# Kernel tuning notes

Hardware: AMD Instinct MI355X
Metric: run time of the kernel (lower is better)

Reference implementation:

```python
import jax, jax.numpy as jnp
import numpy as np

SCALE = 32.0 / 32.0  # alpha / rank
KEEP = 1.0 - 0.05    # dropout keep prob


def setup_inputs() -> dict:
    key = jax.random.key(0)
    kx, kw, ka, kb, km = jax.random.split(key, 5)
    B_, S, D_in, D_out, R = 4, 2048, 4096, 4096, 32
    x = jax.random.normal(kx, (B_, S, D_in), dtype=jnp.float32)
    W = jax.random.normal(kw, (D_out, D_in), dtype=jnp.float32) * (1.0 / np.sqrt(D_in))
    A = jax.random.normal(ka, (D_in, R), dtype=jnp.float32) * (1.0 / np.sqrt(D_in))
    Bm = jax.random.normal(kb, (R, D_out), dtype=jnp.float32) * 0.02
    # deterministic inverted-dropout mask: {0, 1/KEEP}
    drop_mask = (jax.random.uniform(km, (B_, S, D_in)) < KEEP).astype(jnp.float32) / KEEP
    return {"x": x, "W": W, "A": A, "B": Bm, "drop_mask": drop_mask}


def reference(x, W, A, B, drop_mask):
    # base: F.linear(x, W)  -> x @ W.T   [b,s,out]
    base = jnp.einsum("bsi,oi->bso", x, W)
    # lora: dropout(x) @ A @ B, low-rank path (contract rank first)
    lora = jnp.einsum("bsr,ro->bso", jnp.einsum("bsi,ir->bsr", x * drop_mask, A), B)
    return base + SCALE * lora
```

## Files before the change

kernel.cpp:

```cpp
#include <hip/hip_runtime.h>
#include <hip/hip_bf16.h>

typedef short bf16x8 __attribute__((ext_vector_type(8)));
typedef float f32x4  __attribute__((ext_vector_type(4)));

#define DIN  4096
#define DOUT 4096
#define MTOT 8192
#define RNK  32
#define NT   64

union Pk8 { __hip_bfloat16 h[8]; uint4 u; bf16x8 v; };

__device__ __forceinline__ uint4 pack8(float a0,float a1,float a2,float a3,
                                       float b0,float b1,float b2,float b3){
  Pk8 p;
  p.h[0]=__float2bfloat16(a0); p.h[1]=__float2bfloat16(a1);
  p.h[2]=__float2bfloat16(a2); p.h[3]=__float2bfloat16(a3);
  p.h[4]=__float2bfloat16(b0); p.h[5]=__float2bfloat16(b1);
  p.h[6]=__float2bfloat16(b2); p.h[7]=__float2bfloat16(b3);
  return p.u;
}
__device__ __forceinline__ bf16x8 pack8v(float a0,float a1,float a2,float a3,
                                         float b0,float b1,float b2,float b3){
  Pk8 p;
  p.h[0]=__float2bfloat16(a0); p.h[1]=__float2bfloat16(a1);
  p.h[2]=__float2bfloat16(a2); p.h[3]=__float2bfloat16(a3);
  p.h[4]=__float2bfloat16(b0); p.h[5]=__float2bfloat16(b1);
  p.h[6]=__float2bfloat16(b2); p.h[7]=__float2bfloat16(b3);
  return p.v;
}

__device__ __forceinline__ void gload_lds16(const void* g, void* l){
  __builtin_amdgcn_global_load_lds(
      (const __attribute__((address_space(1))) unsigned int*)g,
      (__attribute__((address_space(3))) unsigned int*)l, 16, 0, 0);
}

#define MFMA(A,B,C) __builtin_amdgcn_mfma_f32_16x16x32_bf16(A,B,C,0,0,0)
#define BAR   asm volatile("s_barrier" ::: "memory")
#define PRIO1 __builtin_amdgcn_s_setprio(1)
#define PRIO0 __builtin_amdgcn_s_setprio(0)

__global__ __launch_bounds__(256) void k_conv_w(const float* __restrict__ W,
                                                __hip_bfloat16* __restrict__ Wb){
  size_t i = ((size_t)blockIdx.x*256 + threadIdx.x) * 8;
  float4 a = *(const float4*)(W + i);
  float4 b = *(const float4*)(W + i + 4);
  *(uint4*)(Wb + i) = pack8(a.x,a.y,a.z,a.w,b.x,b.y,b.z,b.w);
}

__global__ __launch_bounds__(256) void k_conv_ab(const float* __restrict__ A,
                                                 const float* __restrict__ B,
                                                 __hip_bfloat16* __restrict__ At,
                                                 __hip_bfloat16* __restrict__ Bt){
  int idx = blockIdx.x*256 + threadIdx.x;
  if (idx < DIN*RNK){
    int k = idx >> 5, r = idx & 31;
    At[(size_t)r*DIN + k] = __float2bfloat16(A[(size_t)k*RNK + r]);
  } else {
    int j = idx - DIN*RNK;
    int n = j >> 5, k = j & 31;
    Bt[(size_t)n*RNK + k] = __float2bfloat16(B[(size_t)k*DOUT + n]);
  }
}

__global__ __launch_bounds__(256) void k_xt(const float* __restrict__ x,
                                            const float* __restrict__ mk,
                                            const __hip_bfloat16* __restrict__ At,
                                            __hip_bfloat16* __restrict__ xb,
                                            __hip_bfloat16* __restrict__ tb){
  __shared__ float sred[4*512];
  const int t = threadIdx.x, w = t >> 6, l = t & 63;
  const int r0 = blockIdx.x * 16;
  const int lane15 = l & 15, kb = l >> 4;
  const size_t rowbase = (size_t)(r0 + lane15) * DIN;
  const int kbase = w * 1024;

  f32x4 acc0 = {0.f,0.f,0.f,0.f}, acc1 = {0.f,0.f,0.f,0.f};
  const __hip_bfloat16* at0 = At + (size_t)lane15*DIN;
  const __hip_bfloat16* at1 = At + (size_t)(16+lane15)*DIN;

  #pragma unroll 2
  for (int kt = 0; kt < 32; ++kt){
    const int k0 = kbase + kt*32 + kb*8;
    float4 xa = *(const float4*)(x  + rowbase + k0);
    float4 xc = *(const float4*)(x  + rowbase + k0 + 4);
    float4 ma = *(const float4*)(mk + rowbase + k0);
    float4 mc = *(const float4*)(mk + rowbase + k0 + 4);
    *(uint4*)(xb + rowbase + k0) = pack8(xa.x,xa.y,xa.z,xa.w,xc.x,xc.y,xc.z,xc.w);
    bf16x8 af = pack8v(xa.x*ma.x,xa.y*ma.y,xa.z*ma.z,xa.w*ma.w,
                       xc.x*mc.x,xc.y*mc.y,xc.z*mc.z,xc.w*mc.w);
    bf16x8 b0 = *(const bf16x8*)(at0 + k0);
    bf16x8 b1 = *(const bf16x8*)(at1 + k0);
    acc0 = MFMA(af, b0, acc0);
    acc1 = MFMA(af, b1, acc1);
  }

  #pragma unroll
  for (int r = 0; r < 4; ++r){
    sred[(w*64+l)*8 + r]     = acc0[r];
    sred[(w*64+l)*8 + 4 + r] = acc1[r];
  }
  __syncthreads();
  #pragma unroll
  for (int e2 = 0; e2 < 2; ++e2){
    int e  = t*2 + e2;
    int el = e >> 3, er = e & 7;
    float s = sred[el*8+er] + sred[512+el*8+er] + sred[1024+el*8+er] + sred[1536+el*8+er];
    int col  = (er>>2)*16 + (el & 15);
    int orow = (el>>4)*4 + (er & 3);
    tb[(size_t)(r0 + orow)*RNK + col] = __float2bfloat16(s);
  }
}

__global__ __launch_bounds__(512, 2) void k_main2(const __hip_bfloat16* __restrict__ xb,
                                                  const __hip_bfloat16* __restrict__ Wb,
                                                  const __hip_bfloat16* __restrict__ tb,
                                                  const __hip_bfloat16* __restrict__ Bt,
                                                  float* __restrict__ out){
  __shared__ __align__(16) __hip_bfloat16 lds[65536];
  const int tid = threadIdx.x;
  const int l  = tid & 63, w = tid >> 6;
  const int wm = w >> 2,  wn = w & 3;
  const int lr = l & 15;
  const int ch = ((l >> 4) ^ ((l >> 1) & 3)) & 3;
  const int laneA = (wm*128 + lr)*32 + ch*8;
  const int laneB = (wn*64  + lr)*32 + ch*8;
  const int g_row = tid >> 2;
  const int g_ch  = (((tid & 3) ^ ((tid >> 3) & 3))) * 8;

  const int bid  = blockIdx.x;
  const int xcd  = bid & 7;
  const int idx  = bid >> 3;
  const int bm0  = (((xcd >> 1) << 3) + (idx & 7)) * 256;
  const int bn0  = (((xcd & 1) << 3) + (idx >> 3)) * 256;

  f32x4 acc[8][4];

  {
    const __hip_bfloat16* tp = tb + (size_t)(bm0 + wm*128 + lr)*RNK + (l>>4)*8;
    const __hip_bfloat16* bp = Bt + (size_t)(bn0 + wn*64  + lr)*RNK + (l>>4)*8;
    bf16x8 tf[8], bf[4];
    #pragma unroll
    for (int m = 0; m < 8; ++m) tf[m] = *(const bf16x8*)(tp + m*16*RNK);
    #pragma unroll
    for (int n = 0; n < 4; ++n) bf[n] = *(const bf16x8*)(bp + n*16*RNK);
    const f32x4 z = {0.f,0.f,0.f,0.f};
    #pragma unroll
    for (int m = 0; m < 8; ++m)
      #pragma unroll
      for (int n = 0; n < 4; ++n)
        acc[m][n] = MFMA(tf[m], bf[n], z);
  }
  asm volatile("" ::: "memory");

  auto STAGE = [&](int bb, int ab, int kh, int kt){
    const __hip_bfloat16* g = ab ? Wb : xb;
    const int base0 = ab ? bn0 : bm0;
    const int segb  = bb*32768 + ab*16384 + kh*8192;
    #pragma unroll
    for (int i = 0; i < 2; ++i){
      const __hip_bfloat16* src = g + (size_t)(base0 + i*128 + g_row)*DIN
                                    + kt*64 + kh*32 + g_ch;
      gload_lds16(src, (void*)&lds[segb + i*4096 + w*512]);
    }
  };

  STAGE(0,1,0,0); STAGE(0,0,0,0); STAGE(0,1,1,0); STAGE(0,0,1,0);
  STAGE(1,1,0,1); STAGE(1,0,0,1); STAGE(1,1,1,1);
  asm volatile("s_waitcnt vmcnt(6)" ::: "memory");
  BAR;

  #define LDV(off) (*(const bf16x8*)&lds[(off)])

  for (int t = 0; t < NT; ++t){
    const int b   = t & 1;
    const int sA0 = b*32768;
    const int sA1 = b*32768 + 8192;
    const int sB0 = b*32768 + 16384;
    const int sB1 = b*32768 + 24576;
    bf16x8 bk0[4], bk1[4];
    bf16x8 a0, a1, a2, a3;

    a0 = LDV(sA0+laneA);        a1 = LDV(sA0+laneA+512);
    a2 = LDV(sA0+laneA+1024);   a3 = LDV(sA0+laneA+1536);
    #pragma unroll
    for (int n = 0; n < 4; ++n) bk0[n] = LDV(sB0+laneB+n*512);
    if (t+1 < NT) STAGE(b^1, 0, 1, t+1);
    BAR;
    PRIO1;
    #pragma unroll
    for (int n = 0; n < 4; ++n){
      acc[0][n] = MFMA(a0, bk0[n], acc[0][n]);
      acc[1][n] = MFMA(a1, bk0[n], acc[1][n]);
      acc[2][n] = MFMA(a2, bk0[n], acc[2][n]);
      acc[3][n] = MFMA(a3, bk0[n], acc[3][n]);
    }
    PRIO0;
    BAR;

    a0 = LDV(sA0+laneA+2048);   a1 = LDV(sA0+laneA+2560);
    a2 = LDV(sA0+laneA+3072);   a3 = LDV(sA0+laneA+3584);
    #pragma unroll
    for (int n = 0; n < 4; ++n) bk1[n] = LDV(sB1+laneB+n*512);
    if (t+2 < NT) STAGE(b, 1, 0, t+2);
    BAR;
    PRIO1;
    #pragma unroll
    for (int n = 0; n < 4; ++n){
      acc[4][n] = MFMA(a0, bk0[n], acc[4][n]);
      acc[5][n] = MFMA(a1, bk0[n], acc[5][n]);
      acc[6][n] = MFMA(a2, bk0[n], acc[6][n]);
      acc[7][n] = MFMA(a3, bk0[n], acc[7][n]);
    }
    PRIO0;
    BAR;

    a0 = LDV(sA1+laneA);        a1 = LDV(sA1+laneA+512);
    a2 = LDV(sA1+laneA+1024);   a3 = LDV(sA1+laneA+1536);
    if (t+2 < NT) STAGE(b, 0, 0, t+2);
    BAR;
    PRIO1;
    #pragma unroll
    for (int n = 0; n < 4; ++n){
      acc[0][n] = MFMA(a0, bk1[n], acc[0][n]);
      acc[1][n] = MFMA(a1, bk1[n], acc[1][n]);
      acc[2][n] = MFMA(a2, bk1[n], acc[2][n]);
      acc[3][n] = MFMA(a3, bk1[n], acc[3][n]);
    }
    PRIO0;
    BAR;

    a0 = LDV(sA1+laneA+2048);   a1 = LDV(sA1+laneA+2560);
    a2 = LDV(sA1+laneA+3072);   a3 = LDV(sA1+laneA+3584);
    if (t+2 < NT) STAGE(b, 1, 1, t+2);
    BAR;
    PRIO1;
    #pragma unroll
    for (int n = 0; n < 4; ++n){
      acc[4][n] = MFMA(a0, bk1[n], acc[4][n]);
      acc[5][n] = MFMA(a1, bk1[n], acc[5][n]);
      acc[6][n] = MFMA(a2, bk1[n], acc[6][n]);
      acc[7][n] = MFMA(a3, bk1[n], acc[7][n]);
    }
    PRIO0;
    if (t < NT-2)       asm volatile("s_waitcnt vmcnt(6)" ::: "memory");
    else if (t == NT-2) asm volatile("s_waitcnt vmcnt(0)" ::: "memory");
    BAR;
  }

  const int orow = bm0 + wm*128 + (l>>4)*4;
  const int ocol = bn0 + wn*64  + (l&15);
  #pragma unroll
  for (int m = 0; m < 8; ++m)
    #pragma unroll
    for (int n = 0; n < 4; ++n)
      #pragma unroll
      for (int r = 0; r < 4; ++r)
        out[(size_t)(orow + m*16 + r)*DOUT + ocol + n*16] = acc[m][n][r];
  #undef LDV
}

__global__ void fb_t(const float* __restrict__ x, const float* __restrict__ mk,
                     const float* __restrict__ A, float* __restrict__ tf){
  const int m = blockIdx.x, t = threadIdx.x;
  float acc[RNK];
  #pragma unroll
  for (int r = 0; r < RNK; ++r) acc[r] = 0.f;
  for (int k = t; k < DIN; k += 256){
    float xm = x[(size_t)m*DIN + k] * mk[(size_t)m*DIN + k];
    #pragma unroll
    for (int r = 0; r < RNK; ++r) acc[r] += xm * A[(size_t)k*RNK + r];
  }
  #pragma unroll
  for (int r = 0; r < RNK; ++r){
    float v = acc[r];
    for (int o = 32; o; o >>= 1) v += __shfl_down(v, o);
    if ((t & 63) == 0) atomicAdd(&tf[(size_t)m*RNK + r], v);
  }
}

__global__ void fb_out(const float* __restrict__ x, const float* __restrict__ W,
                       const float* __restrict__ B, const float* __restrict__ tf,
                       float* __restrict__ out){
  size_t idx = (size_t)blockIdx.x*256 + threadIdx.x;
  int m = (int)(idx >> 12), n = (int)(idx & 4095);
  float acc = 0.f;
  for (int k = 0; k < DIN; ++k)
    acc += x[(size_t)m*DIN + k] * W[(size_t)n*DIN + k];
  #pragma unroll
  for (int r = 0; r < RNK; ++r)
    acc += tf[(size_t)m*RNK + r] * B[(size_t)r*DOUT + n];
  out[idx] = acc;
}

extern "C" void kernel_launch(void* const* d_in, const int* in_sizes, int n_in,
                              void* d_out, int out_size, void* d_ws, size_t ws_size,
                              hipStream_t stream) {
  const float* x  = (const float*)d_in[0];
  const float* W  = (const float*)d_in[1];
  const float* A  = (const float*)d_in[2];
  const float* B  = (const float*)d_in[3];
  const float* mk = (const float*)d_in[4];
  float* out = (float*)d_out;

  const size_t OFF_XB = 0;
  const size_t OFF_WB = OFF_XB + (size_t)MTOT*DIN*2;
  const size_t OFF_TB = OFF_WB + (size_t)DOUT*DIN*2;
  const size_t OFF_AT = OFF_TB + (size_t)MTOT*RNK*2;
  const size_t OFF_BT = OFF_AT + (size_t)RNK*DIN*2;
  const size_t NEED   = OFF_BT + (size_t)DIN*RNK*2;

  if (ws_size >= NEED){
    char* ws = (char*)d_ws;
    __hip_bfloat16* xb = (__hip_bfloat16*)(ws + OFF_XB);
    __hip_bfloat16* Wb = (__hip_bfloat16*)(ws + OFF_WB);
    __hip_bfloat16* tb = (__hip_bfloat16*)(ws + OFF_TB);
    __hip_bfloat16* At = (__hip_bfloat16*)(ws + OFF_AT);
    __hip_bfloat16* Bt = (__hip_bfloat16*)(ws + OFF_BT);

    k_conv_w <<<(DOUT*(size_t)DIN)/(256*8), 256, 0, stream>>>(W, Wb);
    k_conv_ab<<<(2*DIN*RNK)/256,            256, 0, stream>>>(A, B, At, Bt);
    k_xt     <<<MTOT/16,                    256, 0, stream>>>(x, mk, At, xb, tb);
    k_main2  <<<(MTOT/256)*(DOUT/256),      512, 0, stream>>>(xb, Wb, tb, Bt, out);
  } else {
    float* tf = (float*)d_ws;
    hipMemsetAsync(tf, 0, (size_t)MTOT*RNK*4, stream);
    fb_t  <<<MTOT, 256, 0, stream>>>(x, mk, A, tf);
    fb_out<<<((size_t)MTOT*DOUT)/256, 256, 0, stream>>>(x, W, B, tf, out);
  }
}
```

Before: 337.7 us.

## Software-pipeline LDS fragment loads with MFMAs and halve barriers per phase

Restructures the GEMM main loop so A and B fragments are double-buffered in registers (aE/aO, bk0/bk1). Each phase now loads the next phase's fragments from LDS while issuing MFMAs on the current ones, with a single barrier per phase instead of two. The prologue stages the whole second k-tile and preloads the first fragments, and sched_barrier stops the compiler from reordering across phase boundaries. The aim is to hide LDS read latency behind matrix math and cut barrier stalls, at the cost of higher register pressure. The tail waitcnt handling is simplified to an unconditional vmcnt(6), which may not drain the last in-flight tile before it is read.

```diff
diff --git a/kernel.cpp b/kernel.cpp
--- a/kernel.cpp
+++ b/kernel.cpp
@@ -39,6 +39,7 @@
 
 #define MFMA(A,B,C) __builtin_amdgcn_mfma_f32_16x16x32_bf16(A,B,C,0,0,0)
 #define BAR   asm volatile("s_barrier" ::: "memory")
+#define SB0   __builtin_amdgcn_sched_barrier(0)
 #define PRIO1 __builtin_amdgcn_s_setprio(1)
 #define PRIO0 __builtin_amdgcn_s_setprio(0)
 
@@ -167,87 +168,86 @@
     }
   };
 
+  #define ASEG(bb,kh) ((bb)*32768 + (kh)*8192)
+  #define BSEG(bb,kh) ((bb)*32768 + 16384 + (kh)*8192)
+  #define LDV(off) (*(const bf16x8*)&lds[(off)])
+
   STAGE(0,1,0,0); STAGE(0,0,0,0); STAGE(0,1,1,0); STAGE(0,0,1,0);
-  STAGE(1,1,0,1); STAGE(1,0,0,1); STAGE(1,1,1,1);
-  asm volatile("s_waitcnt vmcnt(6)" ::: "memory");
-  BAR;
-
-  #define LDV(off) (*(const bf16x8*)&lds[(off)])
+  STAGE(1,1,0,1); STAGE(1,0,0,1); STAGE(1,1,1,1); STAGE(1,0,1,1);
+  asm volatile("s_waitcnt vmcnt(8)" ::: "memory");
+  BAR; SB0;
+
+  bf16x8 aE[4], aO[4], bk0[4], bk1[4];
+  #pragma unroll
+  for (int i = 0; i < 4; ++i) aE[i] = LDV(ASEG(0,0)+laneA+i*512);
+  #pragma unroll
+  for (int n = 0; n < 4; ++n) bk0[n] = LDV(BSEG(0,0)+laneB+n*512);
 
   for (int t = 0; t < NT; ++t){
-    const int b   = t & 1;
-    const int sA0 = b*32768;
-    const int sA1 = b*32768 + 8192;
-    const int sB0 = b*32768 + 16384;
-    const int sB1 = b*32768 + 24576;
-    bf16x8 bk0[4], bk1[4];
-    bf16x8 a0, a1, a2, a3;
-
-    a0 = LDV(sA0+laneA);        a1 = LDV(sA0+laneA+512);
-    a2 = LDV(sA0+laneA+1024);   a3 = LDV(sA0+laneA+1536);
-    #pragma unroll
-    for (int n = 0; n < 4; ++n) bk0[n] = LDV(sB0+laneB+n*512);
-    if (t+1 < NT) STAGE(b^1, 0, 1, t+1);
-    BAR;
+    const int b = t & 1, bn = b ^ 1;
+
+    BAR; SB0;
+    #pragma unroll
+    for (int i = 0; i < 4; ++i) aO[i] = LDV(ASEG(b,0)+laneA+2048+i*512);
+    #pragma unroll
+    for (int n = 0; n < 4; ++n) bk1[n] = LDV(BSEG(b,1)+laneB+n*512);
+    if (t+2 < NT) STAGE(b, 1, 0, t+2);
     PRIO1;
     #pragma unroll
     for (int n = 0; n < 4; ++n){
-      acc[0][n] = MFMA(a0, bk0[n], acc[0][n]);
-      acc[1][n] = MFMA(a1, bk0[n], acc[1][n]);
-      acc[2][n] = MFMA(a2, bk0[n], acc[2][n]);
-      acc[3][n] = MFMA(a3, bk0[n], acc[3][n]);
+      acc[0][n] = MFMA(aE[0], bk0[n], acc[0][n]);
+      acc[1][n] = MFMA(aE[1], bk0[n], acc[1][n]);
+      acc[2][n] = MFMA(aE[2], bk0[n], acc[2][n]);
+      acc[3][n] = MFMA(aE[3], bk0[n], acc[3][n]);
     }
     PRIO0;
-    BAR;
-
-    a0 = LDV(sA0+laneA+2048);   a1 = LDV(sA0+laneA+2560);
-    a2 = LDV(sA0+laneA+3072);   a3 = LDV(sA0+laneA+3584);
-    #pragma unroll
-    for (int n = 0; n < 4; ++n) bk1[n] = LDV(sB1+laneB+n*512);
-    if (t+2 < NT) STAGE(b, 1, 0, t+2);
-    BAR;
+
+    BAR; SB0;
+    #pragma unroll
+    for (int i = 0; i < 4; ++i) aE[i] = LDV(ASEG(b,1)+laneA+i*512);
+    if (t+2 < NT) STAGE(b, 0, 0, t+2);
     PRIO1;
     #pragma unroll
     for (int n = 0; n < 4; ++n){
-      acc[4][n] = MFMA(a0, bk0[n], acc[4][n]);
-      acc[5][n] = MFMA(a1, bk0[n], acc[5][n]);
-      acc[6][n] = MFMA(a2, bk0[n], acc[6][n]);
-      acc[7][n] = MFMA(a3, bk0[n], acc[7][n]);
+      acc[4][n] = MFMA(aO[0], bk0[n], acc[4][n]);
+      acc[5][n] = MFMA(aO[1], bk0[n], acc[5][n]);
+      acc[6][n] = MFMA(aO[2], bk0[n], acc[6][n]);
+      acc[7][n] = MFMA(aO[3], bk0[n], acc[7][n]);
     }
     PRIO0;
-    BAR;
-
-    a0 = LDV(sA1+laneA);        a1 = LDV(sA1+laneA+512);
-    a2 = LDV(sA1+laneA+1024);   a3 = LDV(sA1+laneA+1536);
-    if (t+2 < NT) STAGE(b, 0, 0, t+2);
-    BAR;
+
+    BAR; SB0;
+    #pragma unroll
+    for (int i = 0; i < 4; ++i) aO[i] = LDV(ASEG(b,1)+laneA+2048+i*512);
+    if (t+2 < NT) STAGE(b, 1, 1, t+2);
     PRIO1;
     #pragma unroll
     for (int n = 0; n < 4; ++n){
-      acc[0][n] = MFMA(a0, bk1[n], acc[0][n]);
-      acc[1][n] = MFMA(a1, bk1[n], acc[1][n]);
-      acc[2][n] = MFMA(a2, bk1[n], acc[2][n]);
-      acc[3][n] = MFMA(a3, bk1[n], acc[3][n]);
+      acc[0][n] = MFMA(aE[0], bk1[n], acc[0][n]);
+      acc[1][n] = MFMA(aE[1], bk1[n], acc[1][n]);
+      acc[2][n] = MFMA(aE[2], bk1[n], acc[2][n]);
+      acc[3][n] = MFMA(aE[3], bk1[n], acc[3][n]);
     }
     PRIO0;
-    BAR;
-
-    a0 = LDV(sA1+laneA+2048);   a1 = LDV(sA1+laneA+2560);
-    a2 = LDV(sA1+laneA+3072);   a3 = LDV(sA1+laneA+3584);
-    if (t+2 < NT) STAGE(b, 1, 1, t+2);
-    BAR;
+    asm volatile("s_waitcnt vmcnt(6)" ::: "memory");
+
+    BAR; SB0;
+    if (t+1 < NT){
+      #pragma unroll
+      for (int i = 0; i < 4; ++i) aE[i] = LDV(ASEG(bn,0)+laneA+i*512);
+      #pragma unroll
+      for (int n = 0; n < 4; ++n) bk0[n] = LDV(BSEG(bn,0)+laneB+n*512);
+    }
+    if (t+2 < NT) STAGE(b, 0, 1, t+2);
     PRIO1;
     #pragma unroll
     for (int n = 0; n < 4; ++n){
-      acc[4][n] = MFMA(a0, bk1[n], acc[4][n]);
-      acc[5][n] = MFMA(a1, bk1[n], acc[5][n]);
-      acc[6][n] = MFMA(a2, bk1[n], acc[6][n]);
-      acc[7][n] = MFMA(a3, bk1[n], acc[7][n]);
+      acc[4][n] = MFMA(aO[0], bk1[n], acc[4][n]);
+      acc[5][n] = MFMA(aO[1], bk1[n], acc[5][n]);
+      acc[6][n] = MFMA(aO[2], bk1[n], acc[6][n]);
+      acc[7][n] = MFMA(aO[3], bk1[n], acc[7][n]);
     }
     PRIO0;
-    if (t < NT-2)       asm volatile("s_waitcnt vmcnt(6)" ::: "memory");
-    else if (t == NT-2) asm volatile("s_waitcnt vmcnt(0)" ::: "memory");
-    BAR;
   }
 
   const int orow = bm0 + wm*128 + (l>>4)*4;
@@ -260,6 +260,8 @@
       for (int r = 0; r < 4; ++r)
         out[(size_t)(orow + m*16 + r)*DOUT + ocol + n*16] = acc[m][n][r];
   #undef LDV
+  #undef ASEG
+  #undef BSEG
 }
 
 __global__ void fb_t(const float* __restrict__ x, const float* __restrict__ mk,
```

After: 337.2 us. Within noise of the previous version (-0.1%).

## Restructure main GEMM into 8-phase pipeline with new LDS swizzle and quadrant MFMA

Applied to the files above, without the earlier changes.

Rewrites the main bf16 GEMM loop to process two K-tiles per iteration as eight phases. Each phase computes one quadrant of the accumulator tile with full K=64 per LDS tile, and global-to-LDS staging is interleaved one segment per phase. The LDS layout changes to 64-element rows with an XOR swizzle across 8 chunks to cut bank conflicts. Explicit lgkmcnt/vmcnt waits and sched_barrier fences control instruction ordering. This adds more barriers per K-tile and keeps more fragments live in registers, which raises register pressure and tightens the prefetch-distance accounting.

```diff
diff --git a/kernel.cpp b/kernel.cpp
--- a/kernel.cpp
+++ b/kernel.cpp
@@ -9,6 +9,7 @@
 #define MTOT 8192
 #define RNK  32
 #define NT   64
+#define NT2  32
 
 union Pk8 { __hip_bfloat16 h[8]; uint4 u; bf16x8 v; };
 
@@ -39,6 +40,7 @@
 
 #define MFMA(A,B,C) __builtin_amdgcn_mfma_f32_16x16x32_bf16(A,B,C,0,0,0)
 #define BAR   asm volatile("s_barrier" ::: "memory")
+#define SB0   __builtin_amdgcn_sched_barrier(0)
 #define PRIO1 __builtin_amdgcn_s_setprio(1)
 #define PRIO0 __builtin_amdgcn_s_setprio(0)
 
@@ -114,7 +116,7 @@
   }
 }
 
-__global__ __launch_bounds__(512, 2) void k_main2(const __hip_bfloat16* __restrict__ xb,
+__global__ __launch_bounds__(512, 2) void k_main3(const __hip_bfloat16* __restrict__ xb,
                                                   const __hip_bfloat16* __restrict__ Wb,
                                                   const __hip_bfloat16* __restrict__ tb,
                                                   const __hip_bfloat16* __restrict__ Bt,
@@ -123,12 +125,13 @@
   const int tid = threadIdx.x;
   const int l  = tid & 63, w = tid >> 6;
   const int wm = w >> 2,  wn = w & 3;
-  const int lr = l & 15;
-  const int ch = ((l >> 4) ^ ((l >> 1) & 3)) & 3;
-  const int laneA = (wm*128 + lr)*32 + ch*8;
-  const int laneB = (wn*64  + lr)*32 + ch*8;
-  const int g_row = tid >> 2;
-  const int g_ch  = (((tid & 3) ^ ((tid >> 3) & 3))) * 8;
+  const int lr = l & 15, kb = l >> 4;
+  const int cSwz = (l & 7) ^ ((l >> 3) & 7);
+  const int pc   = lr*64 + (kb ^ (lr & 3))*8;
+  const int khp0 = ((lr >> 2) & 1) * 32;
+  const int khp1 = 32 - khp0;
+  const int aBase = wm*8192;
+  const int bBase = 16384 + wn*4096;
 
   const int bid  = blockIdx.x;
   const int xcd  = bid & 7;
@@ -139,8 +142,8 @@
   f32x4 acc[8][4];
 
   {
-    const __hip_bfloat16* tp = tb + (size_t)(bm0 + wm*128 + lr)*RNK + (l>>4)*8;
-    const __hip_bfloat16* bp = Bt + (size_t)(bn0 + wn*64  + lr)*RNK + (l>>4)*8;
+    const __hip_bfloat16* tp = tb + (size_t)(bm0 + wm*128 + lr)*RNK + kb*8;
+    const __hip_bfloat16* bp = Bt + (size_t)(bn0 + wn*64  + lr)*RNK + kb*8;
     bf16x8 tf[8], bf[4];
     #pragma unroll
     for (int m = 0; m < 8; ++m) tf[m] = *(const bf16x8*)(tp + m*16*RNK);
@@ -155,98 +158,63 @@
   }
   asm volatile("" ::: "memory");
 
-  auto STAGE = [&](int bb, int ab, int kh, int kt){
+  auto STAGE = [&](int buf, int ab, int h, int kt){
     const __hip_bfloat16* g = ab ? Wb : xb;
     const int base0 = ab ? bn0 : bm0;
-    const int segb  = bb*32768 + ab*16384 + kh*8192;
+    const int seg = buf*32768 + ab*16384 + h*8192;
     #pragma unroll
     for (int i = 0; i < 2; ++i){
-      const __hip_bfloat16* src = g + (size_t)(base0 + i*128 + g_row)*DIN
-                                    + kt*64 + kh*32 + g_ch;
-      gload_lds16(src, (void*)&lds[segb + i*4096 + w*512]);
+      const int row = i*64 + w*8 + (l >> 3);
+      const __hip_bfloat16* src = g + (size_t)(base0 + h*128 + row)*DIN
+                                    + kt*64 + cSwz*8;
+      gload_lds16(src, (void*)&lds[seg + i*4096 + w*512]);
     }
   };
 
-  STAGE(0,1,0,0); STAGE(0,0,0,0); STAGE(0,1,1,0); STAGE(0,0,1,0);
-  STAGE(1,1,0,1); STAGE(1,0,0,1); STAGE(1,1,1,1);
-  asm volatile("s_waitcnt vmcnt(6)" ::: "memory");
+  #define LDV(off) (*(const bf16x8*)&lds[(off)])
+  #define RDA(dst, buf, mq) { _Pragma("unroll") for (int i4=0;i4<4;++i4){ \
+      dst[i4][0] = LDV((buf)*32768 + aBase + ((mq)*4+i4)*1024 + pc + khp0); \
+      dst[i4][1] = LDV((buf)*32768 + aBase + ((mq)*4+i4)*1024 + pc + khp1); } }
+  #define RDB(dst, buf, nq) { _Pragma("unroll") for (int j2=0;j2<2;++j2){ \
+      dst[j2][0] = LDV((buf)*32768 + bBase + ((nq)*2+j2)*1024 + pc + khp0); \
+      dst[j2][1] = LDV((buf)*32768 + bBase + ((nq)*2+j2)*1024 + pc + khp1); } }
+  #define MM(mq, nq, A_, B_) { PRIO1; _Pragma("unroll") for (int kh=0;kh<2;++kh) \
+      _Pragma("unroll") for (int i4=0;i4<4;++i4) _Pragma("unroll") for (int j2=0;j2<2;++j2) \
+        acc[(mq)*4+i4][(nq)*2+j2] = MFMA(A_[i4][kh], B_[j2][kh], acc[(mq)*4+i4][(nq)*2+j2]); \
+      PRIO0; }
+  #define PH_OPEN BAR; asm volatile("s_waitcnt lgkmcnt(0)" ::: "memory"); SB0
+
+  STAGE(0,1,0,0); STAGE(0,1,1,0); STAGE(0,0,0,0); STAGE(0,0,1,0);
+  STAGE(1,1,0,1); STAGE(1,1,1,1);
+  asm volatile("s_waitcnt vmcnt(4)" ::: "memory");
   BAR;
 
-  #define LDV(off) (*(const bf16x8*)&lds[(off)])
-
-  for (int t = 0; t < NT; ++t){
-    const int b   = t & 1;
-    const int sA0 = b*32768;
-    const int sA1 = b*32768 + 8192;
-    const int sB0 = b*32768 + 16384;
-    const int sB1 = b*32768 + 24576;
-    bf16x8 bk0[4], bk1[4];
-    bf16x8 a0, a1, a2, a3;
-
-    a0 = LDV(sA0+laneA);        a1 = LDV(sA0+laneA+512);
-    a2 = LDV(sA0+laneA+1024);   a3 = LDV(sA0+laneA+1536);
-    #pragma unroll
-    for (int n = 0; n < 4; ++n) bk0[n] = LDV(sB0+laneB+n*512);
-    if (t+1 < NT) STAGE(b^1, 0, 1, t+1);
+  bf16x8 aX[4][2], aY[4][2], bA[2][2], bB[2][2];
+
+  for (int j = 0; j < NT2; ++j){
+    const int t2 = 2*j;
+    RDA(aX, 0, 0); RDB(bA, 0, 0);
+    STAGE(1, 0, 0, t2+1);
+    asm volatile("s_waitcnt lgkmcnt(8)" ::: "memory");
+    PH_OPEN; MM(0,0,aX,bA); BAR;
+    RDB(bB, 0, 1); STAGE(1, 0, 1, t2+1);
+    PH_OPEN; MM(0,1,aX,bB); BAR;
+    RDA(aY, 0, 1); if (j < NT2-1) STAGE(0, 1, 0, t2+2);
+    PH_OPEN; MM(1,0,aY,bA);
+    if (j < NT2-1) asm volatile("s_waitcnt vmcnt(2)" ::: "memory");
+    else           asm volatile("s_waitcnt vmcnt(0)" ::: "memory");
     BAR;
-    PRIO1;
-    #pragma unroll
-    for (int n = 0; n < 4; ++n){
-      acc[0][n] = MFMA(a0, bk0[n], acc[0][n]);
-      acc[1][n] = MFMA(a1, bk0[n], acc[1][n]);
-      acc[2][n] = MFMA(a2, bk0[n], acc[2][n]);
-      acc[3][n] = MFMA(a3, bk0[n], acc[3][n]);
-    }
-    PRIO0;
-    BAR;
-
-    a0 = LDV(sA0+laneA+2048);   a1 = LDV(sA0+laneA+2560);
-    a2 = LDV(sA0+laneA+3072);   a3 = LDV(sA0+laneA+3584);
-    #pragma unroll
-    for (int n = 0; n < 4; ++n) bk1[n] = LDV(sB1+laneB+n*512);
-    if (t+2 < NT) STAGE(b, 1, 0, t+2);
-    BAR;
-    PRIO1;
-    #pragma unroll
-    for (int n = 0; n < 4; ++n){
-      acc[4][n] = MFMA(a0, bk0[n], acc[4][n]);
-      acc[5][n] = MFMA(a1, bk0[n], acc[5][n]);
-      acc[6][n] = MFMA(a2, bk0[n], acc[6][n]);
-      acc[7][n] = MFMA(a3, bk0[n], acc[7][n]);
-    }
-    PRIO0;
-    BAR;
-
-    a0 = LDV(sA1+laneA);        a1 = LDV(sA1+laneA+512);
-    a2 = LDV(sA1+laneA+1024);   a3 = LDV(sA1+laneA+1536);
-    if (t+2 < NT) STAGE(b, 0, 0, t+2);
-    BAR;
-    PRIO1;
-    #pragma unroll
-    for (int n = 0; n < 4; ++n){
-      acc[0][n] = MFMA(a0, bk1[n], acc[0][n]);
-      acc[1][n] = MFMA(a1, bk1[n], acc[1][n]);
-      acc[2][n] = MFMA(a2, bk1[n], acc[2][n]);
-      acc[3][n] = MFMA(a3, bk1[n], acc[3][n]);
-    }
-    PRIO0;
-    BAR;
-
-    a0 = LDV(sA1+laneA+2048);   a1 = LDV(sA1+laneA+2560);
-    a2 = LDV(sA1+laneA+3072);   a3 = LDV(sA1+laneA+3584);
-    if (t+2 < NT) STAGE(b, 1, 1, t+2);
-    BAR;
-    PRIO1;
-    #pragma unroll
-    for (int n = 0; n < 4; ++n){
-      acc[4][n] = MFMA(a0, bk1[n], acc[4][n]);
-      acc[5][n] = MFMA(a1, bk1[n], acc[5][n]);
-      acc[6][n] = MFMA(a2, bk1[n], acc[6][n]);
-      acc[7][n] = MFMA(a3, bk1[n], acc[7][n]);
-    }
-    PRIO0;
-    if (t < NT-2)       asm volatile("s_waitcnt vmcnt(6)" ::: "memory");
-    else if (t == NT-2) asm volatile("s_waitcnt vmcnt(0)" ::: "memory");
+    RDA(aX, 1, 0); if (j < NT2-1) STAGE(0, 1, 1, t2+2);
+    PH_OPEN; MM(1,1,aY,bB); BAR;
+    RDB(bA, 1, 0); if (j < NT2-1) STAGE(0, 0, 0, t2+2);
+    PH_OPEN; MM(0,0,aX,bA); BAR;
+    RDB(bB, 1, 1); if (j < NT2-1) STAGE(0, 0, 1, t2+2);
+    PH_OPEN; MM(0,1,aX,bB); BAR;
+    RDA(aY, 1, 1); if (j < NT2-1) STAGE(1, 1, 0, t2+3);
+    PH_OPEN; MM(1,0,aY,bA); BAR;
+    if (j < NT2-1) STAGE(1, 1, 1, t2+3);
+    PH_OPEN; MM(1,1,aY,bB);
+    if (j < NT2-1) asm volatile("s_waitcnt vmcnt(4)" ::: "memory");
     BAR;
   }
 
@@ -260,6 +228,10 @@
       for (int r = 0; r < 4; ++r)
         out[(size_t)(orow + m*16 + r)*DOUT + ocol + n*16] = acc[m][n][r];
   #undef LDV
+  #undef RDA
+  #undef RDB
+  #undef MM
+  #undef PH_OPEN
 }
 
 __global__ void fb_t(const float* __restrict__ x, const float* __restrict__ mk,
@@ -323,7 +295,7 @@
     k_conv_w <<<(DOUT*(size_t)DIN)/(256*8), 256, 0, stream>>>(W, Wb);
     k_conv_ab<<<(2*DIN*RNK)/256,            256, 0, stream>>>(A, B, At, Bt);
     k_xt     <<<MTOT/16,                    256, 0, stream>>>(x, mk, At, xb, tb);
-    k_main2  <<<(MTOT/256)*(DOUT/256),      512, 0, stream>>>(xb, Wb, tb, Bt, out);
+    k_main3  <<<(MTOT/256)*(DOUT/256),      512, 0, stream>>>(xb, Wb, tb, Bt, out);
   } else {
     float* tf = (float*)d_ws;
     hipMemsetAsync(tf, 0, (size_t)MTOT*RNK*4, stream);
```

New measurement: 428.1 us. +26.8%, slower.
